# Performance work log

Measured on AMD Instinct MI355X. Metric: run time of the kernel, lower is better.

Reference implementation:

```python
import jax, jax.numpy as jnp
import numpy as np

DIM = 1024
N_HEADS = 16
N_KV = 4
HEAD_DIM = 64
FFN = 4096
EPS = 1e-6
B, S = 2, 2048
ROPE_BASE = 10000.0


def rmsnorm(x, w, eps=EPS):
    ms = jnp.mean(jnp.square(x), axis=-1, keepdims=True)
    return x * jax.lax.rsqrt(ms + eps) * w


def apply_rotary(x, cos, sin):
    # x: [B,H,S,hd]; cos/sin: [S, hd//2] -> broadcast over B,H
    half = x.shape[-1] // 2
    x1, x2 = x[..., :half], x[..., half:]
    c = cos[None, None, :, :]
    s = sin[None, None, :, :]
    return jnp.concatenate((x1 * c + x2 * s, x2 * c - x1 * s), axis=-1)


def setup_inputs() -> dict:
    key = jax.random.key(0)
    ks = jax.random.split(key, 10)
    w = lambda k, shp: jax.random.normal(k, shp, dtype=jnp.float32) * 0.02
    pos = jnp.arange(S, dtype=jnp.float32)
    inv_freq = 1.0 / (ROPE_BASE ** (jnp.arange(0, HEAD_DIM // 2, dtype=jnp.float32) / (HEAD_DIM // 2)))
    ang = pos[:, None] * inv_freq[None, :]
    return {
        "x": jax.random.normal(ks[0], (B, S, DIM), dtype=jnp.float32),
        "w_norm1": jnp.ones((DIM,), jnp.float32),
        "wq": w(ks[1], (DIM, N_HEADS * HEAD_DIM)),
        "wk": w(ks[2], (DIM, N_KV * HEAD_DIM)),
        "wv": w(ks[3], (DIM, N_KV * HEAD_DIM)),
        "wo": w(ks[4], (N_HEADS * HEAD_DIM, DIM)),
        "attn_scale": jnp.ones((DIM,), jnp.float32),
        "w_norm2": jnp.ones((DIM,), jnp.float32),
        "wg": w(ks[5], (DIM, FFN)),
        "wu": w(ks[6], (DIM, FFN)),
        "wd": w(ks[7], (FFN, DIM)),
        "mlp_scale": jnp.ones((DIM,), jnp.float32),
        "cos": jnp.cos(ang),
        "sin": jnp.sin(ang),
    }


def block_forward(x, w_norm1, wq, wk, wv, wo, attn_scale, w_norm2, wg, wu, wd, mlp_scale, cos, sin):
    b, s, d = x.shape
    # ---- attention sub-block (pre-norm, RoPE, causal GQA SDPA, scaled residual) ----
    xn = rmsnorm(x, w_norm1)
    q = (xn @ wq).reshape(b, s, N_HEADS, HEAD_DIM).transpose(0, 2, 1, 3)  # [B,H,S,hd]
    k = (xn @ wk).reshape(b, s, N_KV, HEAD_DIM).transpose(0, 2, 1, 3)    # [B,KV,S,hd]
    v = (xn @ wv).reshape(b, s, N_KV, HEAD_DIM).transpose(0, 2, 1, 3)
    q = apply_rotary(q, cos, sin)
    k = apply_rotary(k, cos, sin)
    rep = N_HEADS // N_KV
    k = jnp.repeat(k, rep, axis=1)  # GQA expand -> [B,H,S,hd]
    v = jnp.repeat(v, rep, axis=1)
    scale = 1.0 / np.sqrt(HEAD_DIM)
    scores = jnp.einsum("bhqd,bhkd->bhqk", q, k) * scale
    causal = jnp.tril(jnp.ones((s, s), dtype=bool))
    scores = jnp.where(causal[None, None], scores, jnp.finfo(scores.dtype).min)
    probs = jax.nn.softmax(scores, axis=-1)
    attn = jnp.einsum("bhqk,bhkd->bhqd", probs, v)
    attn = attn.transpose(0, 2, 1, 3).reshape(b, s, N_HEADS * HEAD_DIM)
    x = x + (attn @ wo) * attn_scale[None, None, :]
    # ---- MLP sub-block (pre-norm, fused gate/up SwiGLU, down proj, scaled residual) ----
    xn2 = rmsnorm(x, w_norm2)
    hidden = jax.nn.silu(xn2 @ wg) * (xn2 @ wu)  # SwiGLU
    x = x + (hidden @ wd) * mlp_scale[None, None, :]
    return x


def reference(x, w_norm1, wq, wk, wv, wo, attn_scale, w_norm2, wg, wu, wd, mlp_scale, cos, sin):
    return block_forward(x, w_norm1, wq, wk, wv, wo, attn_scale, w_norm2, wg, wu, wd, mlp_scale, cos, sin)
```

## Files before the change

kernel.cpp:

```cpp
#include <hip/hip_runtime.h>
#include <hip/hip_bf16.h>
#include <cstdint>

typedef unsigned short u16;
typedef unsigned int u32;
typedef __attribute__((ext_vector_type(4))) float f32x4;
typedef __attribute__((ext_vector_type(8))) __bf16 bf16x8;

#define NH 16
#define NKV 4
#define SEQ 2048
#define NTOK 4096

__device__ inline u16 f2bf(float f) {
  return __builtin_bit_cast(u16, __float2bfloat16(f));
}
__device__ inline float bf2f(u16 u) {
  return __bfloat162float(__builtin_bit_cast(__hip_bfloat16, u));
}

#define GLDS(gp, lp) __builtin_amdgcn_global_load_lds( \
    (__attribute__((address_space(1))) void*)(gp), \
    (__attribute__((address_space(3))) void*)(lp), 16, 0, 0)

#define VMCNT0 asm volatile("s_waitcnt vmcnt(0)" ::: "memory")

__global__ __launch_bounds__(256) void rmsnorm_kernel(
    const float* __restrict__ x, const float* __restrict__ w,
    u16* __restrict__ out) {
  int row = blockIdx.x;
  int tid = threadIdx.x;
  const float4 v = reinterpret_cast<const float4*>(x + (size_t)row * 1024)[tid];
  float ss = v.x * v.x + v.y * v.y + v.z * v.z + v.w * v.w;
#pragma unroll
  for (int off = 32; off; off >>= 1) ss += __shfl_xor(ss, off);
  __shared__ float red[4];
  int lane = tid & 63, wid = tid >> 6;
  if (lane == 0) red[wid] = ss;
  __syncthreads();
  float tot = red[0] + red[1] + red[2] + red[3];
  float r = rsqrtf(tot * (1.0f / 1024.0f) + 1e-6f);
  const float4 wv = reinterpret_cast<const float4*>(w)[tid];
  ushort4 o;
  o.x = f2bf(v.x * r * wv.x);
  o.y = f2bf(v.y * r * wv.y);
  o.z = f2bf(v.z * r * wv.z);
  o.w = f2bf(v.w * r * wv.w);
  reinterpret_cast<ushort4*>(out + (size_t)row * 1024)[tid] = o;
}

__global__ __launch_bounds__(256) void transpose_cast_kernel(
    const float* __restrict__ src, u16* __restrict__ dst, int K, int N) {
  __shared__ float tile[32][33];
  int n0 = blockIdx.x * 32, k0 = blockIdx.y * 32;
  int tx = threadIdx.x & 31, ty = threadIdx.x >> 5;
#pragma unroll
  for (int i = 0; i < 4; i++)
    tile[ty + i * 8][tx] = src[(size_t)(k0 + ty + i * 8) * N + n0 + tx];
  __syncthreads();
#pragma unroll
  for (int i = 0; i < 4; i++)
    dst[(size_t)(n0 + ty + i * 8) * K + k0 + tx] = f2bf(tile[tx][ty + i * 8]);
}

template <int EP>
__device__ inline void epi_store(float v, size_t idx, int col,
                                 float* __restrict__ outf,
                                 const float* __restrict__ res,
                                 const float* __restrict__ scale,
                                 u16* __restrict__ outb) {
  if (EP == 0) {
    outf[idx] = v;
  } else if (EP == 1) {
    outf[idx] = res[idx] + v * scale[col];
  } else if (EP == 2) {
    outb[idx] = f2bf(v / (1.0f + __expf(-v)));
  } else {
    outb[idx] = f2bf(bf2f(outb[idx]) * v);
  }
}

template <int EP>
__global__ __launch_bounds__(256, 1) void gemmB(
    const u16* __restrict__ A, const u16* __restrict__ Bt,
    int M, int N, int K,
    float* __restrict__ outf, const float* __restrict__ res,
    const float* __restrict__ scale, u16* __restrict__ outb) {
  __shared__ u16 SA[2][128 * 64];
  __shared__ u16 SB[2][128 * 64];
  const int tid = threadIdx.x, lane = tid & 63, w = tid >> 6;
  const int wr = w >> 1, wc = w & 1;
  const int lg = lane >> 4, lc = lane & 15, cx = lc & 7;

  const int r8 = blockIdx.x & 7, j = blockIdx.x >> 3;
  const int bm = ((r8 << 2) + (j & 3)) << 7;
  const int bn = (j >> 2) << 7;

  const int swrow = lane >> 3;
  const int swcol = (lane & 7) ^ swrow;
  const u16* gA = A + (size_t)(bm + w * 32 + swrow) * K + swcol * 8;
  const u16* gB = Bt + (size_t)(bn + w * 32 + swrow) * K + swcol * 8;

  const int NT = K >> 6;
  f32x4 acc[4][4] = {};

#define SG2(T_) do { int sl_ = (T_) & 1; size_t ko_ = (size_t)(T_) * 64; \
    GLDS(gA + ko_,                   &SA[sl_][(w * 32) * 64]); \
    GLDS(gA + ko_ + (size_t)8 * K,   &SA[sl_][(w * 32 + 8) * 64]); \
    GLDS(gA + ko_ + (size_t)16 * K,  &SA[sl_][(w * 32 + 16) * 64]); \
    GLDS(gA + ko_ + (size_t)24 * K,  &SA[sl_][(w * 32 + 24) * 64]); \
    GLDS(gB + ko_,                   &SB[sl_][(w * 32) * 64]); \
    GLDS(gB + ko_ + (size_t)8 * K,   &SB[sl_][(w * 32 + 8) * 64]); \
    GLDS(gB + ko_ + (size_t)16 * K,  &SB[sl_][(w * 32 + 16) * 64]); \
    GLDS(gB + ko_ + (size_t)24 * K,  &SB[sl_][(w * 32 + 24) * 64]); } while (0)

  SG2(0);
  VMCNT0;
  __builtin_amdgcn_s_barrier();

  for (int t = 0; t < NT; ++t) {
    const u16* sa = &SA[t & 1][0];
    const u16* sb = &SB[t & 1][0];
    const bool more = (t + 1 < NT);

    bf16x8 bfr[4][2], afr[4][2];
#pragma unroll
    for (int n = 0; n < 4; n++) {
      const int row = wc * 64 + n * 16 + lc;
#pragma unroll
      for (int ks = 0; ks < 2; ks++)
        bfr[n][ks] = *reinterpret_cast<const bf16x8*>(
            &sb[row * 64 + ((((ks << 2) | lg) ^ cx) << 3)]);
    }
#pragma unroll
    for (int i = 0; i < 4; i++) {
      const int row = wr * 64 + i * 16 + lc;
#pragma unroll
      for (int ks = 0; ks < 2; ks++)
        afr[i][ks] = *reinterpret_cast<const bf16x8*>(
            &sa[row * 64 + ((((ks << 2) | lg) ^ cx) << 3)]);
    }
    if (more) SG2(t + 1);
    __builtin_amdgcn_s_setprio(1);
#pragma unroll
    for (int i = 0; i < 4; i++)
#pragma unroll
      for (int n = 0; n < 4; n++) {
        acc[i][n] = __builtin_amdgcn_mfma_f32_16x16x32_bf16(afr[i][0], bfr[n][0], acc[i][n], 0, 0, 0);
        acc[i][n] = __builtin_amdgcn_mfma_f32_16x16x32_bf16(afr[i][1], bfr[n][1], acc[i][n], 0, 0, 0);
      }
    __builtin_amdgcn_s_setprio(0);
    VMCNT0;
    __builtin_amdgcn_s_barrier();
  }
#undef SG2

#pragma unroll
  for (int mi = 0; mi < 4; mi++)
#pragma unroll
    for (int ni = 0; ni < 4; ni++)
#pragma unroll
      for (int rg = 0; rg < 4; rg++) {
        const int row = bm + wr * 64 + mi * 16 + lg * 4 + rg;
        const int col = bn + wc * 64 + ni * 16 + lc;
        epi_store<EP>(acc[mi][ni][rg], (size_t)row * N + col, col, outf, res, scale, outb);
      }
}

__global__ __launch_bounds__(512, 1) void gateup_kernel(
    const u16* __restrict__ A, const u16* __restrict__ Bg,
    const u16* __restrict__ Bu, u16* __restrict__ outb) {
  const int K = 1024, N = 4096;
  __shared__ u16 SA[2][128 * 64];
  __shared__ u16 SG[2][128 * 64];
  __shared__ u16 SU[2][128 * 64];
  const int tid = threadIdx.x, lane = tid & 63, w = tid >> 6;
  const int wr = w >> 2, wc = w & 3;
  const int lg = lane >> 4, lc = lane & 15, cx = lc & 7;

  const int r8 = blockIdx.x & 7, j = blockIdx.x >> 3;
  const int bm = ((r8 >> 1) * 8 + (j & 7)) << 7;
  const int bn = ((r8 & 1) * 16 + (j >> 3)) << 7;

  const int swrow = lane >> 3;
  const int swcol = (lane & 7) ^ swrow;
  const u16* gAs = A + (size_t)(bm + w * 16 + swrow) * K + swcol * 8;
  const u16* gGs = Bg + (size_t)(bn + w * 16 + swrow) * K + swcol * 8;
  const u16* gUs = Bu + (size_t)(bn + w * 16 + swrow) * K + swcol * 8;

  f32x4 accG[4][2] = {}, accU[4][2] = {};

#define SGU(T_) do { int sl_ = (T_) & 1; size_t ko_ = (size_t)(T_) * 64; \
    GLDS(gAs + ko_,                  &SA[sl_][(w * 16) * 64]); \
    GLDS(gAs + ko_ + (size_t)8 * K,  &SA[sl_][(w * 16 + 8) * 64]); \
    GLDS(gGs + ko_,                  &SG[sl_][(w * 16) * 64]); \
    GLDS(gGs + ko_ + (size_t)8 * K,  &SG[sl_][(w * 16 + 8) * 64]); \
    GLDS(gUs + ko_,                  &SU[sl_][(w * 16) * 64]); \
    GLDS(gUs + ko_ + (size_t)8 * K,  &SU[sl_][(w * 16 + 8) * 64]); } while (0)

  SGU(0);
  VMCNT0;
  __builtin_amdgcn_s_barrier();

  for (int t = 0; t < 16; ++t) {
    const u16* sa = &SA[t & 1][0];
    const u16* sg = &SG[t & 1][0];
    const u16* su = &SU[t & 1][0];
    const bool more = (t + 1 < 16);

    bf16x8 afr[4][2], gfr[2][2], ufr[2][2];
#pragma unroll
    for (int i = 0; i < 4; i++) {
      const int row = wr * 64 + i * 16 + lc;
#pragma unroll
      for (int ks = 0; ks < 2; ks++)
        afr[i][ks] = *reinterpret_cast<const bf16x8*>(
            &sa[row * 64 + ((((ks << 2) | lg) ^ cx) << 3)]);
    }
#pragma unroll
    for (int n = 0; n < 2; n++) {
      const int row = wc * 32 + n * 16 + lc;
#pragma unroll
      for (int ks = 0; ks < 2; ks++) {
        const int off = row * 64 + ((((ks << 2) | lg) ^ cx) << 3);
        gfr[n][ks] = *reinterpret_cast<const bf16x8*>(&sg[off]);
        ufr[n][ks] = *reinterpret_cast<const bf16x8*>(&su[off]);
      }
    }
    if (more) SGU(t + 1);
    __builtin_amdgcn_s_setprio(1);
#pragma unroll
    for (int i = 0; i < 4; i++)
#pragma unroll
      for (int n = 0; n < 2; n++)
#pragma unroll
        for (int ks = 0; ks < 2; ks++) {
          accG[i][n] = __builtin_amdgcn_mfma_f32_16x16x32_bf16(afr[i][ks], gfr[n][ks], accG[i][n], 0, 0, 0);
          accU[i][n] = __builtin_amdgcn_mfma_f32_16x16x32_bf16(afr[i][ks], ufr[n][ks], accU[i][n], 0, 0, 0);
        }
    __builtin_amdgcn_s_setprio(0);
    VMCNT0;
    __builtin_amdgcn_s_barrier();
  }
#undef SGU

#pragma unroll
  for (int mi = 0; mi < 4; mi++)
#pragma unroll
    for (int ni = 0; ni < 2; ni++)
#pragma unroll
      for (int rg = 0; rg < 4; rg++) {
        const int row = bm + wr * 64 + mi * 16 + lg * 4 + rg;
        const int col = bn + wc * 32 + ni * 16 + lc;
        const float g = accG[mi][ni][rg];
        const float u = accU[mi][ni][rg];
        outb[(size_t)row * N + col] = f2bf((g / (1.0f + __expf(-g))) * u);
      }
}

__global__ __launch_bounds__(256) void rope_kernel(
    const float* __restrict__ qkv, const float* __restrict__ cosb,
    const float* __restrict__ sinb, u16* __restrict__ qr, u16* __restrict__ kr) {
  int idx = blockIdx.x * 256 + threadIdx.x;
  int d = idx & 31;
  int t = idx >> 5;
  int head = t % 20;
  int bs = t / 20;
  int s = bs & (SEQ - 1);
  int b = bs >> 11;
  const float* row = qkv + (size_t)bs * 1536;
  float c = cosb[s * 32 + d], sn = sinb[s * 32 + d];
  const float QSC = 0.18033688011112042f;
  float x1, x2;
  if (head < 16) {
    x1 = row[head * 64 + d];
    x2 = row[head * 64 + d + 32];
    size_t o = ((size_t)(b * NH + head) * SEQ + s) * 64 + d;
    qr[o] = f2bf((x1 * c + x2 * sn) * QSC);
    qr[o + 32] = f2bf((x2 * c - x1 * sn) * QSC);
  } else {
    int kh = head - 16;
    x1 = row[1024 + kh * 64 + d];
    x2 = row[1024 + kh * 64 + d + 32];
    size_t o = ((size_t)(b * NKV + kh) * SEQ + s) * 64 + d;
    kr[o] = f2bf(x1 * c + x2 * sn);
    kr[o + 32] = f2bf(x2 * c - x1 * sn);
  }
}

__global__ __launch_bounds__(256) void vtrans_kernel(
    const float* __restrict__ qkv, u16* __restrict__ vt) {
  int blk = blockIdx.x;
  int st = blk & 31; blk >>= 5;
  int kvh = blk & 3; blk >>= 2;
  int b = blk;
  __shared__ u16 tile[64][65];
  int tx = threadIdx.x & 63;
  int ty = threadIdx.x >> 6;
  int s0 = st * 64;
#pragma unroll
  for (int i = 0; i < 16; i++) {
    int sl = i * 4 + ty;
    tile[sl][tx] = f2bf(qkv[(size_t)(b * SEQ + s0 + sl) * 1536 + 1280 + kvh * 64 + tx]);
  }
  __syncthreads();
  size_t vbase = (size_t)(b * NKV + kvh) * 64 * SEQ;
#pragma unroll
  for (int i = 0; i < 16; i++) {
    int dd = i * 4 + ty;
    vt[vbase + (size_t)dd * SEQ + s0 + tx] = tile[tx][dd];
  }
}

__global__ __launch_bounds__(512, 1) void attn_kernel(
    const u16* __restrict__ qr, const u16* __restrict__ kr,
    const u16* __restrict__ vt, u16* __restrict__ out) {
  __shared__ u16 Ks[2][64 * 64];
  __shared__ u16 Vs[2][64 * 64];
  __shared__ u16 Ps[8][32 * 64];

  const int n = blockIdx.x;
  const int g = n & 7;
  const int b = g >> 2, kvh = g & 3;
  const int h = kvh * 4 + ((n >> 3) & 3);
  const int j = n >> 5;

  const int tid = threadIdx.x;
  const int lane = tid & 63, w = tid >> 6;
  const int lg = lane >> 4, lc = lane & 15;
  const int lc7 = lc & 7;

  const int isH = (w ^ (w >> 2)) & 1;
  const int strip = isH ? (15 - j) : j;
  const int q0w = strip * 128 + (w >> 1) * 32;
  const int nt = 2 * (15 - j) + 2;

  bf16x8 qf[2][2];
  {
    const u16* qp = qr + ((size_t)(b * NH + h) * SEQ + q0w + lc) * 64 + lg * 8;
#pragma unroll
    for (int qt = 0; qt < 2; qt++) {
      qf[qt][0] = *reinterpret_cast<const bf16x8*>(qp + qt * 16 * 64);
      qf[qt][1] = *reinterpret_cast<const bf16x8*>(qp + qt * 16 * 64 + 32);
    }
  }
  VMCNT0;

  const int srow = lane >> 3;
  const int scw = ((lane & 7) ^ srow) << 3;
  const u16* ksrc = kr + (size_t)(b * NKV + kvh) * SEQ * 64 + (size_t)(w * 8 + srow) * 64 + scw;
  const u16* vsrc = vt + ((size_t)(b * NKV + kvh) * 64 + w * 8 + srow) * SEQ + scw;
  u16* Pw = &Ps[w][0];

#define STAGEA(bufi, t) do { \
    GLDS(ksrc + (size_t)(t) * 64 * 64, &Ks[bufi][(w * 8) * 64]); \
    GLDS(vsrc + (size_t)(t) * 64,      &Vs[bufi][(w * 8) * 64]); \
  } while (0)

  STAGEA(0, 0);

  float mm[2] = {-1e30f, -1e30f}, ll[2] = {0.0f, 0.0f};
  f32x4 oacc[2][4] = {};

  int buf = 0;
  for (int t = 0; t < nt; ++t) {
    if (t + 1 < nt) {
      STAGEA(buf ^ 1, t + 1);
      asm volatile("s_waitcnt vmcnt(2)" ::: "memory");
    } else {
      VMCNT0;
    }
    __builtin_amdgcn_s_barrier();
    __builtin_amdgcn_sched_barrier(0);

    const int c0 = t * 64;
    if (c0 <= q0w + 31) {
      bf16x8 kf[4][2];
#pragma unroll
      for (int ni = 0; ni < 4; ni++) {
        const int row = ni * 16 + lc;
#pragma unroll
        for (int hf = 0; hf < 2; hf++)
          kf[ni][hf] = *reinterpret_cast<const bf16x8*>(
              &Ks[buf][row * 64 + ((((hf * 64 + lg * 16)) ^ (lc7 << 4)) >> 1)]);
      }
      f32x4 sc[4][2] = {};
      __builtin_amdgcn_s_setprio(1);
#pragma unroll
      for (int ni = 0; ni < 4; ni++)
#pragma unroll
        for (int qt = 0; qt < 2; qt++) {
          sc[ni][qt] = __builtin_amdgcn_mfma_f32_16x16x32_bf16(kf[ni][0], qf[qt][0], sc[ni][qt], 0, 0, 0);
          sc[ni][qt] = __builtin_amdgcn_mfma_f32_16x16x32_bf16(kf[ni][1], qf[qt][1], sc[ni][qt], 0, 0, 0);
        }
      __builtin_amdgcn_s_setprio(0);
      bf16x8 vf[4][2];
#pragma unroll
      for (int dt = 0; dt < 4; dt++) {
        const int row = dt * 16 + lc;
#pragma unroll
        for (int ks = 0; ks < 2; ks++)
          vf[dt][ks] = *reinterpret_cast<const bf16x8*>(
              &Vs[buf][row * 64 + (((ks * 64 + lg * 16) ^ (lc7 << 4)) >> 1)]);
      }
      if (c0 + 63 > q0w) {
#pragma unroll
        for (int qt = 0; qt < 2; qt++) {
          const int q = q0w + qt * 16 + lc;
#pragma unroll
          for (int ni = 0; ni < 4; ni++)
#pragma unroll
            for (int rg = 0; rg < 4; rg++)
              if (c0 + ni * 16 + lg * 4 + rg > q) sc[ni][qt][rg] = -1e30f;
        }
      }
      float mx[2];
#pragma unroll
      for (int qt = 0; qt < 2; qt++) {
        float v = -1e30f;
#pragma unroll
        for (int ni = 0; ni < 4; ni++)
#pragma unroll
          for (int rg = 0; rg < 4; rg++) v = fmaxf(v, sc[ni][qt][rg]);
        v = fmaxf(v, __shfl_xor(v, 16));
        v = fmaxf(v, __shfl_xor(v, 32));
        mx[qt] = v;
      }
      if (!__all(mx[0] - mm[0] <= 11.5f && mx[1] - mm[1] <= 11.5f)) {
        float al[2];
#pragma unroll
        for (int qt = 0; qt < 2; qt++) {
          float mn = fmaxf(mm[qt], mx[qt]);
          al[qt] = exp2f(mm[qt] - mn);
          mm[qt] = mn;
          ll[qt] *= al[qt];
        }
#pragma unroll
        for (int qt = 0; qt < 2; qt++)
#pragma unroll
          for (int rg = 0; rg < 4; rg++) {
            float a = __shfl(al[qt], lg * 4 + rg);
#pragma unroll
            for (int dt = 0; dt < 4; dt++) oacc[qt][dt][rg] *= a;
          }
      }
#pragma unroll
      for (int qt = 0; qt < 2; qt++) {
        float rs = 0.0f;
#pragma unroll
        for (int ni = 0; ni < 4; ni++)
#pragma unroll
          for (int rg = 0; rg < 4; rg++) {
            float p = exp2f(sc[ni][qt][rg] - mm[qt]);
            sc[ni][qt][rg] = p;
            rs += p;
          }
        rs += __shfl_xor(rs, 16);
        rs += __shfl_xor(rs, 32);
        ll[qt] += rs;
      }
#pragma unroll
      for (int qt = 0; qt < 2; qt++)
#pragma unroll
        for (int ni = 0; ni < 4; ni++) {
          ushort4 pk;
          pk.x = f2bf(sc[ni][qt][0]);
          pk.y = f2bf(sc[ni][qt][1]);
          pk.z = f2bf(sc[ni][qt][2]);
          pk.w = f2bf(sc[ni][qt][3]);
          *reinterpret_cast<ushort4*>(
              &Pw[(qt * 16 + lc) * 64 + (((ni * 32 + lg * 8) ^ (lc7 << 4)) >> 1)]) = pk;
        }
      __builtin_amdgcn_s_setprio(1);
#pragma unroll
      for (int qt = 0; qt < 2; qt++)
#pragma unroll
        for (int ks = 0; ks < 2; ks++) {
          bf16x8 pa = *reinterpret_cast<const bf16x8*>(
              &Pw[(qt * 16 + lc) * 64 + (((ks * 64 + lg * 16) ^ (lc7 << 4)) >> 1)]);
#pragma unroll
          for (int dt = 0; dt < 4; dt++)
            oacc[qt][dt] = __builtin_amdgcn_mfma_f32_16x16x32_bf16(pa, vf[dt][ks], oacc[qt][dt], 0, 0, 0);
        }
      __builtin_amdgcn_s_setprio(0);
    }
    asm volatile("s_waitcnt lgkmcnt(0)" ::: "memory");
    __builtin_amdgcn_s_barrier();
    __builtin_amdgcn_sched_barrier(0);
    buf ^= 1;
  }
#undef STAGEA

#pragma unroll
  for (int qt = 0; qt < 2; qt++) {
    const float li = 1.0f / ll[qt];
#pragma unroll
    for (int rg = 0; rg < 4; rg++) {
      float liq = __shfl(li, lg * 4 + rg);
      int q = q0w + qt * 16 + lg * 4 + rg;
      u16* orow = out + (size_t)(b * SEQ + q) * 1024 + h * 64 + lc;
#pragma unroll
      for (int dt = 0; dt < 4; dt++)
        orow[dt * 16] = f2bf(oacc[qt][dt][rg] * liq);
    }
  }
}

extern "C" void kernel_launch(void* const* d_in, const int* in_sizes, int n_in,
                              void* d_out, int out_size, void* d_ws, size_t ws_size,
                              hipStream_t stream) {
  const float* x = (const float*)d_in[0];
  const float* w_norm1 = (const float*)d_in[1];
  const float* wq = (const float*)d_in[2];
  const float* wk = (const float*)d_in[3];
  const float* wv = (const float*)d_in[4];
  const float* wo = (const float*)d_in[5];
  const float* attn_scale = (const float*)d_in[6];
  const float* w_norm2 = (const float*)d_in[7];
  const float* wg = (const float*)d_in[8];
  const float* wu = (const float*)d_in[9];
  const float* wd = (const float*)d_in[10];
  const float* mlp_scale = (const float*)d_in[11];
  const float* cosb = (const float*)d_in[12];
  const float* sinb = (const float*)d_in[13];
  float* out = (float*)d_out;

  char* ws = (char*)d_ws;
  u16* wqkv_t = (u16*)(ws + 0);
  u16* wo_t = (u16*)(ws + 3145728);
  u16* wg_t = (u16*)(ws + 5242880);
  u16* wu_t = (u16*)(ws + 13631488);
  u16* wd_t = (u16*)(ws + 22020096);
  u16* xn = (u16*)(ws + 30408704);
  float* qkv = (float*)(ws + 38797312);
  u16* attn_o = (u16*)(ws + 38797312);
  float* x1 = (float*)(ws + 47185920);
  u16* q_rope = (u16*)(ws + 63963136);
  u16* k_rope = (u16*)(ws + 72351744);
  u16* vt = (u16*)(ws + 74448896);
  u16* hbuf = (u16*)(ws + 63963136);

  dim3 tb(256);
  transpose_cast_kernel<<<dim3(32, 32), tb, 0, stream>>>(wq, wqkv_t, 1024, 1024);
  transpose_cast_kernel<<<dim3(8, 32), tb, 0, stream>>>(wk, wqkv_t + (size_t)1024 * 1024, 1024, 256);
  transpose_cast_kernel<<<dim3(8, 32), tb, 0, stream>>>(wv, wqkv_t + (size_t)1280 * 1024, 1024, 256);
  transpose_cast_kernel<<<dim3(32, 32), tb, 0, stream>>>(wo, wo_t, 1024, 1024);
  transpose_cast_kernel<<<dim3(128, 32), tb, 0, stream>>>(wg, wg_t, 1024, 4096);
  transpose_cast_kernel<<<dim3(128, 32), tb, 0, stream>>>(wu, wu_t, 1024, 4096);
  transpose_cast_kernel<<<dim3(32, 128), tb, 0, stream>>>(wd, wd_t, 4096, 1024);

  rmsnorm_kernel<<<4096, tb, 0, stream>>>(x, w_norm1, xn);
  gemmB<0><<<dim3(384), dim3(256), 0, stream>>>(xn, wqkv_t, 4096, 1536, 1024, qkv, nullptr, nullptr, nullptr);
  rope_kernel<<<10240, tb, 0, stream>>>(qkv, cosb, sinb, q_rope, k_rope);
  vtrans_kernel<<<2 * 4 * 32, tb, 0, stream>>>(qkv, vt);
  attn_kernel<<<256, dim3(512), 0, stream>>>(q_rope, k_rope, vt, attn_o);
  gemmB<1><<<dim3(256), dim3(256), 0, stream>>>(attn_o, wo_t, 4096, 1024, 1024, x1, x, attn_scale, nullptr);
  rmsnorm_kernel<<<4096, tb, 0, stream>>>(x1, w_norm2, xn);
  gateup_kernel<<<dim3(1024), dim3(512), 0, stream>>>(xn, wg_t, wu_t, hbuf);
  gemmB<1><<<dim3(256), dim3(256), 0, stream>>>(hbuf, wd_t, 4096, 1024, 4096, out, x1, mlp_scale, nullptr);
}
```

Before: 269.8 us.

## Restructure gate/up GEMM into 256x128 tiles with four-phase interleaved staging

The fused gate/up SwiGLU GEMM moves from 128x128 tiles (1024 blocks) to 256-row M tiles (512 blocks), so each gate/up weight tile is reused across twice as many rows. Each K-step is split into four phases, one per half of the M tile and per gate or up. The loads for the next tiles are issued in quarters between these phases, and a partial vmcnt wait keeps prefetches in flight. This aims to cut global traffic and hide load latency, at the cost of more barriers per step, twice the accumulator registers and a tighter launch-bounds occupancy hint.

Result: no change. 269.1 us (-0.3%).

```diff
diff --git a/kernel.cpp b/kernel.cpp
--- a/kernel.cpp
+++ b/kernel.cpp
@@ -24,6 +24,7 @@
     (__attribute__((address_space(3))) void*)(lp), 16, 0, 0)
 
 #define VMCNT0 asm volatile("s_waitcnt vmcnt(0)" ::: "memory")
+#define VMCNT6 asm volatile("s_waitcnt vmcnt(6)" ::: "memory")
 
 __global__ __launch_bounds__(256) void rmsnorm_kernel(
     const float* __restrict__ x, const float* __restrict__ w,
@@ -167,51 +168,55 @@
       }
 }
 
-__global__ __launch_bounds__(512, 1) void gateup_kernel(
+__global__ __launch_bounds__(512, 2) void gateup_kernel(
     const u16* __restrict__ A, const u16* __restrict__ Bg,
     const u16* __restrict__ Bu, u16* __restrict__ outb) {
-  const int K = 1024, N = 4096;
-  __shared__ u16 SA[2][128 * 64];
-  __shared__ u16 SG[2][128 * 64];
-  __shared__ u16 SU[2][128 * 64];
+  const int K = 1024, N = 4096, NT = 16;
+  __shared__ u16 SA[2][256 * 64];
+  __shared__ u16 SB[2][256 * 64];
   const int tid = threadIdx.x, lane = tid & 63, w = tid >> 6;
   const int wr = w >> 2, wc = w & 3;
   const int lg = lane >> 4, lc = lane & 15, cx = lc & 7;
 
   const int r8 = blockIdx.x & 7, j = blockIdx.x >> 3;
-  const int bm = ((r8 >> 1) * 8 + (j & 7)) << 7;
-  const int bn = ((r8 & 1) * 16 + (j >> 3)) << 7;
+  const int bm = (((r8 >> 1) << 2) + (j & 3)) << 8;
+  const int bn = ((r8 & 1) * 16 + (j >> 2)) << 7;
 
   const int swrow = lane >> 3;
   const int swcol = (lane & 7) ^ swrow;
-  const u16* gAs = A + (size_t)(bm + w * 16 + swrow) * K + swcol * 8;
-  const u16* gGs = Bg + (size_t)(bn + w * 16 + swrow) * K + swcol * 8;
-  const u16* gUs = Bu + (size_t)(bn + w * 16 + swrow) * K + swcol * 8;
-
-  f32x4 accG[4][2] = {}, accU[4][2] = {};
-
-#define SGU(T_) do { int sl_ = (T_) & 1; size_t ko_ = (size_t)(T_) * 64; \
-    GLDS(gAs + ko_,                  &SA[sl_][(w * 16) * 64]); \
-    GLDS(gAs + ko_ + (size_t)8 * K,  &SA[sl_][(w * 16 + 8) * 64]); \
-    GLDS(gGs + ko_,                  &SG[sl_][(w * 16) * 64]); \
-    GLDS(gGs + ko_ + (size_t)8 * K,  &SG[sl_][(w * 16 + 8) * 64]); \
-    GLDS(gUs + ko_,                  &SU[sl_][(w * 16) * 64]); \
-    GLDS(gUs + ko_ + (size_t)8 * K,  &SU[sl_][(w * 16 + 8) * 64]); } while (0)
-
-  SGU(0);
-  VMCNT0;
+  const u16* aA = A + (size_t)(bm + w * 8 + swrow) * K + swcol * 8;
+  const u16* aB = A + (size_t)(bm + 64 + w * 8 + swrow) * K + swcol * 8;
+  const u16* gG = Bg + (size_t)(bn + w * 16 + swrow) * K + swcol * 8;
+  const u16* gU = Bu + (size_t)(bn + w * 16 + swrow) * K + swcol * 8;
+
+#define STAGE_H0(T_) do { int b_ = (T_) & 1; size_t ko_ = (size_t)(T_) * 64; \
+    GLDS(aA + ko_,                  &SA[b_][(w * 8) * 64]); \
+    GLDS(aA + ko_ + (size_t)128 * K, &SA[b_][(128 + w * 8) * 64]); } while (0)
+#define STAGE_H3(T_) do { int b_ = (T_) & 1; size_t ko_ = (size_t)(T_) * 64; \
+    GLDS(aB + ko_,                  &SA[b_][(64 + w * 8) * 64]); \
+    GLDS(aB + ko_ + (size_t)128 * K, &SA[b_][(192 + w * 8) * 64]); } while (0)
+#define STAGE_H1(T_) do { int b_ = (T_) & 1; size_t ko_ = (size_t)(T_) * 64; \
+    GLDS(gG + ko_,                 &SB[b_][(w * 16) * 64]); \
+    GLDS(gG + ko_ + (size_t)8 * K, &SB[b_][(w * 16 + 8) * 64]); } while (0)
+#define STAGE_H2(T_) do { int b_ = (T_) & 1; size_t ko_ = (size_t)(T_) * 64; \
+    GLDS(gU + ko_,                 &SB[b_][(128 + w * 16) * 64]); \
+    GLDS(gU + ko_ + (size_t)8 * K, &SB[b_][(128 + w * 16 + 8) * 64]); } while (0)
+
+  f32x4 accG[8][2] = {}, accU[8][2] = {};
+
+  STAGE_H0(0); STAGE_H1(0); STAGE_H2(0); STAGE_H3(0);
+  STAGE_H0(1); STAGE_H1(1); STAGE_H2(1);
+  VMCNT6;
   __builtin_amdgcn_s_barrier();
 
-  for (int t = 0; t < 16; ++t) {
+  for (int t = 0; t < NT; ++t) {
     const u16* sa = &SA[t & 1][0];
-    const u16* sg = &SG[t & 1][0];
-    const u16* su = &SU[t & 1][0];
-    const bool more = (t + 1 < 16);
-
+    const u16* sb = &SB[t & 1][0];
     bf16x8 afr[4][2], gfr[2][2], ufr[2][2];
+
 #pragma unroll
     for (int i = 0; i < 4; i++) {
-      const int row = wr * 64 + i * 16 + lc;
+      const int row = wr * 128 + i * 16 + lc;
 #pragma unroll
       for (int ks = 0; ks < 2; ks++)
         afr[i][ks] = *reinterpret_cast<const bf16x8*>(
@@ -221,36 +226,91 @@
     for (int n = 0; n < 2; n++) {
       const int row = wc * 32 + n * 16 + lc;
 #pragma unroll
-      for (int ks = 0; ks < 2; ks++) {
-        const int off = row * 64 + ((((ks << 2) | lg) ^ cx) << 3);
-        gfr[n][ks] = *reinterpret_cast<const bf16x8*>(&sg[off]);
-        ufr[n][ks] = *reinterpret_cast<const bf16x8*>(&su[off]);
-      }
-    }
-    if (more) SGU(t + 1);
+      for (int ks = 0; ks < 2; ks++)
+        gfr[n][ks] = *reinterpret_cast<const bf16x8*>(
+            &sb[row * 64 + ((((ks << 2) | lg) ^ cx) << 3)]);
+    }
+    if (t + 1 < NT) STAGE_H3(t + 1);
+    __builtin_amdgcn_s_barrier();
     __builtin_amdgcn_s_setprio(1);
 #pragma unroll
     for (int i = 0; i < 4; i++)
 #pragma unroll
       for (int n = 0; n < 2; n++)
 #pragma unroll
-        for (int ks = 0; ks < 2; ks++) {
+        for (int ks = 0; ks < 2; ks++)
           accG[i][n] = __builtin_amdgcn_mfma_f32_16x16x32_bf16(afr[i][ks], gfr[n][ks], accG[i][n], 0, 0, 0);
+    __builtin_amdgcn_s_setprio(0);
+    __builtin_amdgcn_s_barrier();
+
+#pragma unroll
+    for (int n = 0; n < 2; n++) {
+      const int row = 128 + wc * 32 + n * 16 + lc;
+#pragma unroll
+      for (int ks = 0; ks < 2; ks++)
+        ufr[n][ks] = *reinterpret_cast<const bf16x8*>(
+            &sb[row * 64 + ((((ks << 2) | lg) ^ cx) << 3)]);
+    }
+    if (t + 2 < NT) STAGE_H0(t + 2);
+    __builtin_amdgcn_s_barrier();
+    __builtin_amdgcn_s_setprio(1);
+#pragma unroll
+    for (int i = 0; i < 4; i++)
+#pragma unroll
+      for (int n = 0; n < 2; n++)
+#pragma unroll
+        for (int ks = 0; ks < 2; ks++)
           accU[i][n] = __builtin_amdgcn_mfma_f32_16x16x32_bf16(afr[i][ks], ufr[n][ks], accU[i][n], 0, 0, 0);
-        }
     __builtin_amdgcn_s_setprio(0);
-    VMCNT0;
-    __builtin_amdgcn_s_barrier();
-  }
-#undef SGU
-
-#pragma unroll
-  for (int mi = 0; mi < 4; mi++)
+    __builtin_amdgcn_s_barrier();
+
+#pragma unroll
+    for (int i = 0; i < 4; i++) {
+      const int row = wr * 128 + 64 + i * 16 + lc;
+#pragma unroll
+      for (int ks = 0; ks < 2; ks++)
+        afr[i][ks] = *reinterpret_cast<const bf16x8*>(
+            &sa[row * 64 + ((((ks << 2) | lg) ^ cx) << 3)]);
+    }
+    if (t + 2 < NT) STAGE_H1(t + 2);
+    __builtin_amdgcn_s_barrier();
+    __builtin_amdgcn_s_setprio(1);
+#pragma unroll
+    for (int i = 0; i < 4; i++)
+#pragma unroll
+      for (int n = 0; n < 2; n++)
+#pragma unroll
+        for (int ks = 0; ks < 2; ks++)
+          accG[4 + i][n] = __builtin_amdgcn_mfma_f32_16x16x32_bf16(afr[i][ks], gfr[n][ks], accG[4 + i][n], 0, 0, 0);
+    __builtin_amdgcn_s_setprio(0);
+    __builtin_amdgcn_s_barrier();
+
+    if (t + 2 < NT) STAGE_H2(t + 2);
+    if (t < NT - 3) { VMCNT6; } else { VMCNT0; }
+    __builtin_amdgcn_s_barrier();
+    __builtin_amdgcn_s_setprio(1);
+#pragma unroll
+    for (int i = 0; i < 4; i++)
+#pragma unroll
+      for (int n = 0; n < 2; n++)
+#pragma unroll
+        for (int ks = 0; ks < 2; ks++)
+          accU[4 + i][n] = __builtin_amdgcn_mfma_f32_16x16x32_bf16(afr[i][ks], ufr[n][ks], accU[4 + i][n], 0, 0, 0);
+    __builtin_amdgcn_s_setprio(0);
+    __builtin_amdgcn_s_barrier();
+  }
+#undef STAGE_H0
+#undef STAGE_H1
+#undef STAGE_H2
+#undef STAGE_H3
+
+#pragma unroll
+  for (int mi = 0; mi < 8; mi++)
 #pragma unroll
     for (int ni = 0; ni < 2; ni++)
 #pragma unroll
       for (int rg = 0; rg < 4; rg++) {
-        const int row = bm + wr * 64 + mi * 16 + lg * 4 + rg;
+        const int row = bm + wr * 128 + ((mi < 4) ? mi * 16 : 64 + (mi - 4) * 16) + lg * 4 + rg;
         const int col = bn + wc * 32 + ni * 16 + lc;
         const float g = accG[mi][ni][rg];
         const float u = accU[mi][ni][rg];
@@ -556,6 +616,6 @@
   attn_kernel<<<256, dim3(512), 0, stream>>>(q_rope, k_rope, vt, attn_o);
   gemmB<1><<<dim3(256), dim3(256), 0, stream>>>(attn_o, wo_t, 4096, 1024, 1024, x1, x, attn_scale, nullptr);
   rmsnorm_kernel<<<4096, tb, 0, stream>>>(x1, w_norm2, xn);
-  gateup_kernel<<<dim3(1024), dim3(512), 0, stream>>>(xn, wg_t, wu_t, hbuf);
+  gateup_kernel<<<dim3(512), dim3(512), 0, stream>>>(xn, wg_t, wu_t, hbuf);
   gemmB<1><<<dim3(256), dim3(256), 0, stream>>>(hbuf, wd_t, 4096, 1024, 4096, out, x1, mlp_scale, nullptr);
 }
```
